# Optimization experiments

Measured on AMD Instinct MI355X. Metric: run time of the kernel, lower is better.

## Reference

```python
import jax, jax.numpy as jnp
import numpy as np

D_MODEL = 1024
N_HEADS = 16
D_KEYS = 64
D_LLM = 4096
Q_RANK = 512
KV_RANK = 512
EPS = 1e-5


def layernorm(x, g, b):
    mu = jnp.mean(x, axis=-1, keepdims=True)
    var = jnp.mean(jnp.square(x - mu), axis=-1, keepdims=True)
    return (x - mu) * jax.lax.rsqrt(var + EPS) * g + b


def setup_inputs() -> dict:
    key = jax.random.key(0)
    ks = jax.random.split(key, 10)
    te = jax.random.normal(ks[0], (4, 1024, D_MODEL), jnp.float32)
    se = jax.random.normal(ks[1], (1000, D_LLM), jnp.float32)
    s = 0.02
    return {
        'target_embedding': te,
        'source_embedding': se,
        'value_embedding': se,  # module asserts source == value
        'q_a_w': jax.random.normal(ks[2], (Q_RANK, D_MODEL), jnp.float32) * s,
        'q_ln_g': jnp.ones((Q_RANK,), jnp.float32),
        'q_ln_b': jnp.zeros((Q_RANK,), jnp.float32),
        'q_b_w': jax.random.normal(ks[3], (N_HEADS * D_KEYS, Q_RANK), jnp.float32) * s,
        'kv_a_w': jax.random.normal(ks[4], (KV_RANK, D_LLM), jnp.float32) * s,
        'kv_ln_g': jnp.ones((KV_RANK,), jnp.float32),
        'kv_ln_b': jnp.zeros((KV_RANK,), jnp.float32),
        'kv_b_w': jax.random.normal(ks[5], (N_HEADS * 2 * D_KEYS, KV_RANK), jnp.float32) * s,
        'out_w': jax.random.normal(ks[6], (D_LLM, N_HEADS * D_KEYS), jnp.float32) * s,
        'out_b': jnp.zeros((D_LLM,), jnp.float32),
    }


def reference(target_embedding, source_embedding, value_embedding,
              q_a_w, q_ln_g, q_ln_b, q_b_w,
              kv_a_w, kv_ln_g, kv_ln_b, kv_b_w, out_w, out_b):
    B, L, _ = target_embedding.shape
    S = source_embedding.shape[0]
    # Q path: LoRA down -> LN -> up, [B,L,H,E]
    q = layernorm(target_embedding @ q_a_w.T, q_ln_g, q_ln_b) @ q_b_w.T
    q = q.reshape(B, L, N_HEADS, D_KEYS)
    # KV path (no batch dim, broadcast across B)
    ckv = layernorm(source_embedding @ kv_a_w.T, kv_ln_g, kv_ln_b)  # [S, r]
    kv = (ckv @ kv_b_w.T).reshape(S, N_HEADS, 2 * D_KEYS)
    k, v = kv[..., :D_KEYS], kv[..., D_KEYS:]  # [S,H,E] each
    scale = 1.0 / np.sqrt(D_KEYS)
    scores = jnp.einsum('blhe,she->bhls', q, k)  # [B,H,L,S]
    A = jax.nn.softmax(scale * scores, axis=-1)  # dropout inactive (eval)
    out = jnp.einsum('bhls,she->blhe', A, v).reshape(B, L, N_HEADS * D_KEYS)
    return out @ out_w.T + out_b
```

## Files before the change

kernel.cpp:

```cpp
#include <hip/hip_runtime.h>

typedef unsigned short u16;
typedef __bf16 bf16x8 __attribute__((ext_vector_type(8)));
typedef float f32x4 __attribute__((ext_vector_type(4)));

#define DEV __device__ __forceinline__

DEV u16 f2bf(float f){
  unsigned u = __float_as_uint(f);
  u += 0x7fff + ((u >> 16) & 1);
  return (u16)(u >> 16);
}
DEV float bf2f(u16 v){ return __uint_as_float(((unsigned)v) << 16); }

DEV void gll16(const void* g, void* l){
  __builtin_amdgcn_global_load_lds(
    (__attribute__((address_space(1))) unsigned int*)(unsigned long long)g,
    (__attribute__((address_space(3))) unsigned int*)(unsigned int)(unsigned long long)l,
    16, 0, 0);
}

template<int WM, int WN, int OBF, int BIAS>
__global__ __launch_bounds__(256) void gemm_bt(
    const u16* __restrict__ A, int lda, long sA1, long sA2,
    const u16* __restrict__ B, int ldb, long sB1, long sB2,
    void* __restrict__ Cv, int ldc, long sC1, long sC2,
    const float* __restrict__ bias,
    int M, int N, int K, int Z2)
{
  constexpr int BM = WM*64, BN = WN*64;
  constexpr int NW = WM*WN;
  constexpr int A_INSTS = BM/16, B_INSTS = BN/16;
  constexpr int APW = A_INSTS/NW, BPW = B_INSTS/NW;
  __shared__ u16 sA[BM*32];
  __shared__ u16 sB[BN*32];
  const int tid  = threadIdx.x;
  const int wave = tid >> 6, lane = tid & 63;
  const int quad = lane >> 4, l16 = lane & 15;
  const int wm = wave % WM, wn = wave / WM;
  const long bm = blockIdx.y, bn = blockIdx.x;
  const int z  = blockIdx.z;
  const int z1 = z / Z2, z2 = z - z1*Z2;
  const u16* Ab = A + z1*sA1 + z2*sA2 + bm*BM*(long)lda;
  const u16* Bb = B + z1*sB1 + z2*sB2 + bn*BN*(long)ldb;

  f32x4 acc[4][4] = {};

  for (int k0 = 0; k0 < K; k0 += 32){
    __syncthreads();
#pragma unroll
    for (int j = 0; j < APW; j++){
      const int inst = wave*APW + j;
      const int o = inst*1024 + lane*16;
      const int row = o >> 6, colb = o & 63;
      gll16(Ab + (long)row*lda + k0 + (colb >> 1), &sA[inst*512]);
    }
#pragma unroll
    for (int j = 0; j < BPW; j++){
      const int inst = wave*BPW + j;
      const int o = inst*1024 + lane*16;
      const int row = o >> 6, colb = o & 63;
      gll16(Bb + (long)row*ldb + k0 + (colb >> 1), &sB[inst*512]);
    }
    __syncthreads();
    bf16x8 af[4], bfr[4];
#pragma unroll
    for (int mi = 0; mi < 4; mi++)
      af[mi] = *(const bf16x8*)&sA[(wm*64 + mi*16 + l16)*32 + quad*8];
#pragma unroll
    for (int ni = 0; ni < 4; ni++)
      bfr[ni] = *(const bf16x8*)&sB[(wn*64 + ni*16 + l16)*32 + quad*8];
#pragma unroll
    for (int mi = 0; mi < 4; mi++)
#pragma unroll
      for (int ni = 0; ni < 4; ni++)
        acc[mi][ni] = __builtin_amdgcn_mfma_f32_16x16x32_bf16(af[mi], bfr[ni], acc[mi][ni], 0, 0, 0);
  }

  const long crow0 = bm*BM + wm*64 + quad*4;
  const long ccol0 = bn*BN + wn*64 + l16;
  if (OBF){
    u16* Cp = (u16*)Cv + z1*sC1 + z2*sC2;
#pragma unroll
    for (int mi = 0; mi < 4; mi++)
#pragma unroll
      for (int ni = 0; ni < 4; ni++)
#pragma unroll
        for (int r = 0; r < 4; r++)
          Cp[(crow0 + mi*16 + r)*ldc + ccol0 + ni*16] = f2bf(acc[mi][ni][r]);
  } else {
    float* Cp = (float*)Cv + z1*sC1 + z2*sC2;
    float bv[4] = {0.f,0.f,0.f,0.f};
    if (BIAS){
#pragma unroll
      for (int ni = 0; ni < 4; ni++) bv[ni] = bias[ccol0 + ni*16];
    }
#pragma unroll
    for (int mi = 0; mi < 4; mi++)
#pragma unroll
      for (int ni = 0; ni < 4; ni++)
#pragma unroll
        for (int r = 0; r < 4; r++)
          Cp[(crow0 + mi*16 + r)*ldc + ccol0 + ni*16] = acc[mi][ni][r] + bv[ni];
  }
}

__global__ __launch_bounds__(512, 2) void gemm256(
    const u16* __restrict__ A, const u16* __restrict__ B,
    float* __restrict__ C, const float* __restrict__ bias,
    int N, int K, int TN)
{
  __shared__ __align__(16) u16 sA[32768];
  __shared__ __align__(16) u16 sB[32768];
  const int tid  = threadIdx.x;
  const int w    = tid >> 6, lane = tid & 63;
  const int quad = lane >> 4, l16 = lane & 15;
  const int wm = w >> 2, wn = w & 3;
  const int cpx = gridDim.x >> 3;
  const int bid = blockIdx.x;
  const int wg  = (bid & 7)*cpx + (bid >> 3);
  const long bm = wg / TN, bn = wg % TN;
  const int NT = K >> 6;

  const int rsub = lane >> 3;
  const int kk16 = (lane & 7) ^ rsub;
  const u16* Ag = A + (bm*256 + w*8 + rsub)*(long)K + kk16*8;
  const u16* Bg = B + (bn*256 + w*8 + rsub)*(long)K + kk16*8;
  u16* dA = sA + w*512;
  u16* dB = sB + w*512;

  auto stage = [&](const u16* G, u16* D, int T){
#pragma unroll
    for (int c = 0; c < 4; c++)
      gll16(G + ((long)c*64)*K + T*64, D + c*4096);
  };

  const int xr  = l16 & 7;
  const int ko0 = ((0*4 + quad) ^ xr) * 8;
  const int ko1 = ((1*4 + quad) ^ xr) * 8;
  const u16* rA0 = sA + (wm*128 + l16)*64;
  const u16* rB0 = sB + (wn*64  + l16)*64;

  f32x4 acc[8][4] = {};
  bf16x8 aF[4][2];

  stage(Ag, dA, 0);
  stage(Bg, dB, 0);
  asm volatile("s_waitcnt vmcnt(0)" ::: "memory");
  __builtin_amdgcn_s_barrier();

  for (int T = 0; T < NT; ++T){
    const int buf = T & 1;
    const u16* rA = rA0 + buf*16384;
    const u16* rB = rB0 + buf*16384;

    {
#pragma unroll
      for (int mi = 0; mi < 4; mi++){
        aF[mi][0] = *(const bf16x8*)(rA + mi*1024 + ko0);
        aF[mi][1] = *(const bf16x8*)(rA + mi*1024 + ko1);
      }
      bf16x8 bF[2][2];
#pragma unroll
      for (int ni = 0; ni < 2; ni++){
        bF[ni][0] = *(const bf16x8*)(rB + ni*1024 + ko0);
        bF[ni][1] = *(const bf16x8*)(rB + ni*1024 + ko1);
      }
      if (T+1 < NT){
        stage(Ag, dA + (buf^1)*16384, T+1);
        stage(Bg, dB + (buf^1)*16384, T+1);
      }
      __builtin_amdgcn_s_barrier();
      asm volatile("s_waitcnt lgkmcnt(0)" ::: "memory");
      __builtin_amdgcn_sched_barrier(0);
      __builtin_amdgcn_s_setprio(1);
#pragma unroll
      for (int kk = 0; kk < 2; kk++)
#pragma unroll
        for (int mi = 0; mi < 4; mi++)
#pragma unroll
          for (int ni = 0; ni < 2; ni++)
            acc[mi][ni] = __builtin_amdgcn_mfma_f32_16x16x32_bf16(aF[mi][kk], bF[ni][kk], acc[mi][ni], 0,0,0);
      __builtin_amdgcn_s_setprio(0);
      __builtin_amdgcn_s_barrier();
    }

    {
      bf16x8 bF[2][2];
#pragma unroll
      for (int ni = 0; ni < 2; ni++){
        bF[ni][0] = *(const bf16x8*)(rB + (2+ni)*1024 + ko0);
        bF[ni][1] = *(const bf16x8*)(rB + (2+ni)*1024 + ko1);
      }
      __builtin_amdgcn_s_barrier();
      asm volatile("s_waitcnt lgkmcnt(0)" ::: "memory");
      __builtin_amdgcn_sched_barrier(0);
      __builtin_amdgcn_s_setprio(1);
#pragma unroll
      for (int kk = 0; kk < 2; kk++)
#pragma unroll
        for (int mi = 0; mi < 4; mi++)
#pragma unroll
          for (int ni = 0; ni < 2; ni++)
            acc[mi][2+ni] = __builtin_amdgcn_mfma_f32_16x16x32_bf16(aF[mi][kk], bF[ni][kk], acc[mi][2+ni], 0,0,0);
      __builtin_amdgcn_s_setprio(0);
      __builtin_amdgcn_s_barrier();
    }

    {
#pragma unroll
      for (int mi = 0; mi < 4; mi++){
        aF[mi][0] = *(const bf16x8*)(rA + (4+mi)*1024 + ko0);
        aF[mi][1] = *(const bf16x8*)(rA + (4+mi)*1024 + ko1);
      }
      bf16x8 bF[2][2];
#pragma unroll
      for (int ni = 0; ni < 2; ni++){
        bF[ni][0] = *(const bf16x8*)(rB + ni*1024 + ko0);
        bF[ni][1] = *(const bf16x8*)(rB + ni*1024 + ko1);
      }
      __builtin_amdgcn_s_barrier();
      asm volatile("s_waitcnt lgkmcnt(0)" ::: "memory");
      __builtin_amdgcn_sched_barrier(0);
      __builtin_amdgcn_s_setprio(1);
#pragma unroll
      for (int kk = 0; kk < 2; kk++)
#pragma unroll
        for (int mi = 0; mi < 4; mi++)
#pragma unroll
          for (int ni = 0; ni < 2; ni++)
            acc[4+mi][ni] = __builtin_amdgcn_mfma_f32_16x16x32_bf16(aF[mi][kk], bF[ni][kk], acc[4+mi][ni], 0,0,0);
      __builtin_amdgcn_s_setprio(0);
      __builtin_amdgcn_s_barrier();
    }

    {
      bf16x8 bF[2][2];
#pragma unroll
      for (int ni = 0; ni < 2; ni++){
        bF[ni][0] = *(const bf16x8*)(rB + (2+ni)*1024 + ko0);
        bF[ni][1] = *(const bf16x8*)(rB + (2+ni)*1024 + ko1);
      }
      __builtin_amdgcn_s_barrier();
      asm volatile("s_waitcnt lgkmcnt(0)" ::: "memory");
      __builtin_amdgcn_sched_barrier(0);
      __builtin_amdgcn_s_setprio(1);
#pragma unroll
      for (int kk = 0; kk < 2; kk++)
#pragma unroll
        for (int mi = 0; mi < 4; mi++)
#pragma unroll
          for (int ni = 0; ni < 2; ni++)
            acc[4+mi][2+ni] = __builtin_amdgcn_mfma_f32_16x16x32_bf16(aF[mi][kk], bF[ni][kk], acc[4+mi][2+ni], 0,0,0);
      __builtin_amdgcn_s_setprio(0);
      asm volatile("s_waitcnt vmcnt(0)" ::: "memory");
      __builtin_amdgcn_s_barrier();
    }
  }

  const long crow0 = bm*256 + wm*128 + quad*4;
  const long ccol0 = bn*256 + wn*64  + l16;
  float bv[4];
#pragma unroll
  for (int ni = 0; ni < 4; ni++) bv[ni] = bias ? bias[ccol0 + ni*16] : 0.f;
#pragma unroll
  for (int mi = 0; mi < 8; mi++)
#pragma unroll
    for (int ni = 0; ni < 4; ni++)
#pragma unroll
      for (int r = 0; r < 4; r++)
        C[(crow0 + mi*16 + r)*(long)N + ccol0 + ni*16] = acc[mi][ni][r] + bv[ni];
}

__global__ __launch_bounds__(256) void cvt_all(
    const float* __restrict__ te,   const float* __restrict__ qaw,
    const float* __restrict__ qbw,  const float* __restrict__ kvaw,
    const float* __restrict__ kvbw, const float* __restrict__ outw,
    const float* __restrict__ se,
    u16* __restrict__ te_bf, u16* __restrict__ qa_bf, u16* __restrict__ qb_bf,
    u16* __restrict__ kva_bf, u16* __restrict__ kvb_bf,
    u16* __restrict__ outw_bf, u16* __restrict__ se_bf)
{
  const long NG = 4194304;
  for (long g = (long)blockIdx.x*256 + threadIdx.x; g < NG; g += (long)gridDim.x*256){
    const float* src; u16* dst; long rel; bool zero = false;
    if (g < 1048576)      { src=te;   dst=te_bf;   rel=g; }
    else if (g < 1179648) { src=qaw;  dst=qa_bf;   rel=g-1048576; }
    else if (g < 1310720) { src=qbw;  dst=qb_bf;   rel=g-1179648; }
    else if (g < 1835008) { src=kvaw; dst=kva_bf;  rel=g-1310720; }
    else if (g < 2097152) { src=kvbw; dst=kvb_bf;  rel=g-1835008; }
    else if (g < 3145728) { src=outw; dst=outw_bf; rel=g-2097152; }
    else                  { src=se;   dst=se_bf;   rel=g-3145728; zero = (rel>>10) >= 1000; }
    ushort4 o;
    if (!zero){
      float4 v = *(const float4*)(src + rel*4);
      o.x = f2bf(v.x); o.y = f2bf(v.y); o.z = f2bf(v.z); o.w = f2bf(v.w);
    } else { o.x = 0; o.y = 0; o.z = 0; o.w = 0; }
    *(ushort4*)(dst + rel*4) = o;
  }
}

__global__ __launch_bounds__(256) void ln_both(
    u16* __restrict__ out_q,  const float* __restrict__ in_q,
    const float* __restrict__ qg, const float* __restrict__ qb_,
    u16* __restrict__ out_kv, const float* __restrict__ in_kv,
    const float* __restrict__ kg, const float* __restrict__ kb_)
{
  long row; const float* in; u16* outp; const float* gam; const float* bet;
  int nparts; long pstride; int valid;
  if (blockIdx.x < 4096){
    row = blockIdx.x; in = in_q; outp = out_q; gam = qg; bet = qb_;
    nparts = 2; pstride = 4096L*512; valid = 1;
  } else {
    row = blockIdx.x - 4096; in = in_kv; outp = out_kv; gam = kg; bet = kb_;
    nparts = 8; pstride = 1024L*512; valid = (row < 1000);
  }
  const int tid = threadIdx.x;
  u16* op = outp + row*512 + tid*2;
  if (!valid){
    ushort2 z; z.x = 0; z.y = 0;
    *(ushort2*)op = z;
    return;
  }
  float2 x; x.x = 0.f; x.y = 0.f;
  for (int p = 0; p < nparts; p++){
    float2 v = *(const float2*)(in + p*pstride + row*512 + tid*2);
    x.x += v.x; x.y += v.y;
  }
  float s  = x.x + x.y;
  float s2 = x.x*x.x + x.y*x.y;
#pragma unroll
  for (int m = 32; m; m >>= 1){ s += __shfl_xor(s, m, 64); s2 += __shfl_xor(s2, m, 64); }
  __shared__ float red[8];
  const int wave = tid >> 6, lane = tid & 63;
  if (lane == 0){ red[wave*2] = s; red[wave*2+1] = s2; }
  __syncthreads();
  float ts = red[0]+red[2]+red[4]+red[6];
  float t2 = red[1]+red[3]+red[5]+red[7];
  float mu  = ts * (1.f/512.f);
  float var = t2 * (1.f/512.f) - mu*mu;
  float rs  = rsqrtf(var + 1e-5f);
  float2 g2 = *(const float2*)(gam + tid*2);
  float2 b2 = *(const float2*)(bet + tid*2);
  ushort2 o;
  o.x = f2bf((x.x - mu)*rs*g2.x + b2.x);
  o.y = f2bf((x.y - mu)*rs*g2.y + b2.y);
  *(ushort2*)op = o;
}

__global__ __launch_bounds__(256) void split_kv(
    const float* __restrict__ kv, u16* __restrict__ kbf, u16* __restrict__ vT)
{
  const int h  = blockIdx.x;
  const int sc = blockIdx.y;
  const int s0 = sc*64;
  const long PST = 1024L*2048;
  __shared__ u16 tile[64][65];
  const int e  = threadIdx.x & 63;
  const int sg = threadIdx.x >> 6;
#pragma unroll
  for (int i = 0; i < 16; i++){
    const int sl = i*4 + sg;
    const int s = s0 + sl;
    float kvl = kv[(long)s*2048 + h*128 + e]      + kv[PST + (long)s*2048 + h*128 + e];
    float vvl = kv[(long)s*2048 + h*128 + 64 + e] + kv[PST + (long)s*2048 + h*128 + 64 + e];
    kbf[((long)h*1024 + s)*64 + ((e + 8*s) & 63)] = f2bf(kvl);
    tile[sl][e] = f2bf(vvl);
  }
  __syncthreads();
#pragma unroll
  for (int i = 0; i < 16; i++){
    const int er = i*4 + sg;
    const int s  = s0 + e;
    const int t128 = s >> 7, pos = s & 127;
    vT[(((long)h*8 + t128)*64 + er)*128 + ((pos + 8*er) & 127)] = tile[e][er];
  }
}

__global__ __launch_bounds__(256) void flash_attn(
    const u16* __restrict__ Q, const u16* __restrict__ Kt,
    const u16* __restrict__ Vt, u16* __restrict__ O)
{
  __shared__ u16 sKV[128*64];
  __shared__ u16 sPT[128*136];
  __shared__ __align__(16) float sAl[128];
  const int tid = threadIdx.x, w = tid >> 6, lane = tid & 63;
  const int quad = lane >> 4, l16 = lane & 15;
  const int h = blockIdx.y;
  const long q0 = (long)blockIdx.x * 128;

  bf16x8 bq[2][2];
#pragma unroll
  for (int ni = 0; ni < 2; ni++)
#pragma unroll
    for (int kf = 0; kf < 2; kf++)
      bq[ni][kf] = *(const bf16x8*)&Q[(q0 + w*32 + ni*16 + l16)*1024 + h*64 + kf*32 + quad*8];

  f32x4 accO[2][4] = {};
  float mst[2] = {-3e38f, -3e38f};
  float lst[2] = {0.f, 0.f};

  for (int it = 0; it < 8; it++){
    const int s0 = it*128;
    __syncthreads();
#pragma unroll
    for (int j = 0; j < 4; j++){
      const int inst = w*4 + j;
      gll16(Kt + (long)h*65536 + (long)s0*64 + inst*512 + lane*8, &sKV[inst*512]);
    }
    __syncthreads();

    f32x4 accS[8][2] = {};
#pragma unroll
    for (int kf = 0; kf < 2; kf++)
#pragma unroll
      for (int mi = 0; mi < 8; mi++){
        const int sr = mi*16 + l16;
        bf16x8 ka = *(const bf16x8*)&sKV[sr*64 + ((kf*32 + quad*8 + 8*sr) & 63)];
#pragma unroll
        for (int ni = 0; ni < 2; ni++)
          accS[mi][ni] = __builtin_amdgcn_mfma_f32_16x16x32_bf16(ka, bq[ni][kf], accS[mi][ni], 0, 0, 0);
      }

#pragma unroll
    for (int ni = 0; ni < 2; ni++){
      float tm = -3e38f;
#pragma unroll
      for (int mi = 0; mi < 8; mi++)
#pragma unroll
        for (int r = 0; r < 4; r++){
          float v = accS[mi][ni][r] * 0.125f;
          const int s = s0 + mi*16 + quad*4 + r;
          v = (s < 1000) ? v : -3e38f;
          accS[mi][ni][r] = v;
          tm = fmaxf(tm, v);
        }
      tm = fmaxf(tm, __shfl_xor(tm, 16, 64));
      tm = fmaxf(tm, __shfl_xor(tm, 32, 64));
      const float mnew = fmaxf(mst[ni], tm);
      const float al = __expf(mst[ni] - mnew);
      mst[ni] = mnew;
      float sum = 0.f;
      const int qloc = w*32 + ni*16 + l16;
#pragma unroll
      for (int mi = 0; mi < 8; mi++){
        float p0 = __expf(accS[mi][ni][0] - mnew);
        float p1 = __expf(accS[mi][ni][1] - mnew);
        float p2 = __expf(accS[mi][ni][2] - mnew);
        float p3 = __expf(accS[mi][ni][3] - mnew);
        sum += (p0 + p1) + (p2 + p3);
        ushort4 pk;
        pk.x = f2bf(p0); pk.y = f2bf(p1); pk.z = f2bf(p2); pk.w = f2bf(p3);
        *(ushort4*)&sPT[qloc*136 + mi*16 + quad*4] = pk;
      }
      sum += __shfl_xor(sum, 16, 64);
      sum += __shfl_xor(sum, 32, 64);
      lst[ni] = lst[ni]*al + sum;
      if (quad == 0) sAl[qloc] = al;
    }
    __syncthreads();
#pragma unroll
    for (int j = 0; j < 4; j++){
      const int inst = w*4 + j;
      gll16(Vt + ((long)(h*8 + it))*8192 + inst*512 + lane*8, &sKV[inst*512]);
    }
#pragma unroll
    for (int mi = 0; mi < 2; mi++){
      f32x4 al4 = *(const f32x4*)&sAl[w*32 + mi*16 + quad*4];
#pragma unroll
      for (int ni = 0; ni < 4; ni++)
        accO[mi][ni] *= al4;
    }
    __syncthreads();

#pragma unroll
    for (int kf = 0; kf < 4; kf++){
      bf16x8 pa[2], vb[4];
#pragma unroll
      for (int mi = 0; mi < 2; mi++)
        pa[mi] = *(const bf16x8*)&sPT[(w*32 + mi*16 + l16)*136 + kf*32 + quad*8];
#pragma unroll
      for (int ni = 0; ni < 4; ni++){
        const int e = ni*16 + l16;
        vb[ni] = *(const bf16x8*)&sKV[e*128 + ((kf*32 + quad*8 + 8*e) & 127)];
      }
#pragma unroll
      for (int mi = 0; mi < 2; mi++)
#pragma unroll
        for (int ni = 0; ni < 4; ni++)
          accO[mi][ni] = __builtin_amdgcn_mfma_f32_16x16x32_bf16(pa[mi], vb[ni], accO[mi][ni], 0, 0, 0);
    }
  }

  __syncthreads();
  if (quad == 0){ sAl[w*32 + l16] = lst[0]; sAl[w*32 + 16 + l16] = lst[1]; }
  __syncthreads();
#pragma unroll
  for (int mi = 0; mi < 2; mi++){
    f32x4 l4 = *(const f32x4*)&sAl[w*32 + mi*16 + quad*4];
#pragma unroll
    for (int ni = 0; ni < 4; ni++)
#pragma unroll
      for (int r = 0; r < 4; r++)
        O[(q0 + w*32 + mi*16 + quad*4 + r)*1024 + h*64 + ni*16 + l16] =
            f2bf(accO[mi][ni][r] / l4[r]);
  }
}

extern "C" void kernel_launch(void* const* d_in, const int* in_sizes, int n_in,
                              void* d_out, int out_size, void* d_ws, size_t ws_size,
                              hipStream_t stream)
{
  const float* te   = (const float*)d_in[0];
  const float* se   = (const float*)d_in[1];
  const float* qaw  = (const float*)d_in[3];
  const float* qlg  = (const float*)d_in[4];
  const float* qlb  = (const float*)d_in[5];
  const float* qbw  = (const float*)d_in[6];
  const float* kvaw = (const float*)d_in[7];
  const float* kvlg = (const float*)d_in[8];
  const float* kvlb = (const float*)d_in[9];
  const float* kvbw = (const float*)d_in[10];
  const float* outw = (const float*)d_in[11];
  const float* outb = (const float*)d_in[12];
  float* out = (float*)d_out;
  (void)ws_size; (void)in_sizes; (void)n_in; (void)out_size;

  char* ws = (char*)d_ws;
  const size_t MB = 1024*1024;
  u16*   te_bf  = (u16*)  (ws + 0*MB);
  u16*   se_bf  = (u16*)  (ws + 8*MB);
  float* qlat   = (float*)(ws + 16*MB);
  float* ckvp   = (float*)(ws + 32*MB);
  float* kvf    = (float*)(ws + 48*MB);
  u16*   qa_bf   = (u16*)(ws + 64*MB);
  u16*   qb_bf   = (u16*)(ws + 65*MB);
  u16*   kva_bf  = (u16*)(ws + 66*MB);
  u16*   kvb_bf  = (u16*)(ws + 70*MB);
  u16*   outw_bf = (u16*)(ws + 72*MB);
  u16*   qln_bf  = (u16*)(ws + 80*MB);
  u16*   q_bf    = (u16*)(ws + 84*MB);
  u16*   ckv_bf  = (u16*)(ws + 92*MB);
  u16*   k_bf    = (u16*)(ws + 93*MB);
  u16*   vT_bf   = (u16*)(ws + 95*MB);
  u16*   attn_bf = (u16*)(ws + 97*MB);

  cvt_all<<<4096, 256, 0, stream>>>(
      te, qaw, qbw, kvaw, kvbw, outw, se,
      te_bf, qa_bf, qb_bf, kva_bf, kvb_bf, outw_bf, se_bf);

  gemm_bt<2,2,0,0><<<dim3(4, 32, 2), 256, 0, stream>>>(
      te_bf, 1024, 512, 0, qa_bf, 1024, 512, 0,
      qlat, 512, 4096L*512, 0, nullptr, 4096, 512, 512, 1);
  gemm_bt<2,2,0,0><<<dim3(4, 8, 8), 256, 0, stream>>>(
      se_bf, 4096, 512, 0, kva_bf, 4096, 512, 0,
      ckvp, 512, 1024L*512, 0, nullptr, 1024, 512, 512, 1);
  ln_both<<<4096 + 1024, 256, 0, stream>>>(
      qln_bf, qlat, qlg, qlb, ckv_bf, ckvp, kvlg, kvlb);
  gemm_bt<2,2,1,0><<<dim3(8, 32, 1), 256, 0, stream>>>(
      qln_bf, 512, 0,0, qb_bf, 512, 0,0, q_bf, 1024, 0,0, nullptr, 4096, 1024, 512, 1);
  gemm_bt<2,2,0,0><<<dim3(16, 8, 2), 256, 0, stream>>>(
      ckv_bf, 512, 256, 0, kvb_bf, 512, 256, 0,
      kvf, 2048, 1024L*2048, 0, nullptr, 1024, 2048, 256, 1);
  split_kv<<<dim3(16, 16), 256, 0, stream>>>(kvf, k_bf, vT_bf);

  flash_attn<<<dim3(32, 16), 256, 0, stream>>>(q_bf, k_bf, vT_bf, attn_bf);

  gemm256<<<dim3(256), 512, 0, stream>>>(
      attn_bf, outw_bf, out, outb, 4096, 1024, 16);
}
```

Before: 307.6 us.

## Prefetch K and V into separate LDS buffers and use exp2 softmax in attention

Splits the shared K/V staging buffer into separate sK and sV buffers. The next K tile is now loaded asynchronously during the softmax and PV phases of the current tile, and the V tile load is issued before the QK product, which removes two barriers per iteration. The softmax now uses exp2 with log2e folded into the scale, applies the sequence-length mask only on the last tile, and uses a tree max reduction with native bf16 conversion. This costs extra LDS per block and depends on the async LDS loads being properly waited on before the barriers.

After: 313.9 us. +2.0%, slower.

```diff
diff --git a/kernel.cpp b/kernel.cpp
--- a/kernel.cpp
+++ b/kernel.cpp
@@ -2,6 +2,7 @@
 
 typedef unsigned short u16;
 typedef __bf16 bf16x8 __attribute__((ext_vector_type(8)));
+typedef __bf16 bf16x4 __attribute__((ext_vector_type(4)));
 typedef float f32x4 __attribute__((ext_vector_type(4)));
 
 #define DEV __device__ __forceinline__
@@ -381,13 +382,15 @@
     const u16* __restrict__ Q, const u16* __restrict__ Kt,
     const u16* __restrict__ Vt, u16* __restrict__ O)
 {
-  __shared__ u16 sKV[128*64];
+  __shared__ u16 sK[128*64];
+  __shared__ u16 sV[64*128];
   __shared__ u16 sPT[128*136];
   __shared__ __align__(16) float sAl[128];
   const int tid = threadIdx.x, w = tid >> 6, lane = tid & 63;
   const int quad = lane >> 4, l16 = lane & 15;
   const int h = blockIdx.y;
   const long q0 = (long)blockIdx.x * 128;
+  constexpr float SC = 0.18033688011f;
 
   bf16x8 bq[2][2];
 #pragma unroll
@@ -400,15 +403,19 @@
   float mst[2] = {-3e38f, -3e38f};
   float lst[2] = {0.f, 0.f};
 
+#pragma unroll
+  for (int j = 0; j < 4; j++){
+    const int inst = w*4 + j;
+    gll16(Kt + (long)h*65536 + inst*512 + lane*8, &sK[inst*512]);
+  }
+  __syncthreads();
+
   for (int it = 0; it < 8; it++){
-    const int s0 = it*128;
-    __syncthreads();
 #pragma unroll
     for (int j = 0; j < 4; j++){
       const int inst = w*4 + j;
-      gll16(Kt + (long)h*65536 + (long)s0*64 + inst*512 + lane*8, &sKV[inst*512]);
-    }
-    __syncthreads();
+      gll16(Vt + ((long)(h*8 + it))*8192 + inst*512 + lane*8, &sV[inst*512]);
+    }
 
     f32x4 accS[8][2] = {};
 #pragma unroll
@@ -416,54 +423,71 @@
 #pragma unroll
       for (int mi = 0; mi < 8; mi++){
         const int sr = mi*16 + l16;
-        bf16x8 ka = *(const bf16x8*)&sKV[sr*64 + ((kf*32 + quad*8 + 8*sr) & 63)];
+        bf16x8 ka = *(const bf16x8*)&sK[sr*64 + ((kf*32 + quad*8 + 8*sr) & 63)];
 #pragma unroll
         for (int ni = 0; ni < 2; ni++)
           accS[mi][ni] = __builtin_amdgcn_mfma_f32_16x16x32_bf16(ka, bq[ni][kf], accS[mi][ni], 0, 0, 0);
       }
 
+    __syncthreads();
+
+    if (it < 7){
+      const long kb = (long)h*65536 + (long)(it+1)*128*64;
+#pragma unroll
+      for (int j = 0; j < 4; j++){
+        const int inst = w*4 + j;
+        gll16(Kt + kb + inst*512 + lane*8, &sK[inst*512]);
+      }
+    }
+
 #pragma unroll
     for (int ni = 0; ni < 2; ni++){
-      float tm = -3e38f;
 #pragma unroll
       for (int mi = 0; mi < 8; mi++)
 #pragma unroll
-        for (int r = 0; r < 4; r++){
-          float v = accS[mi][ni][r] * 0.125f;
-          const int s = s0 + mi*16 + quad*4 + r;
-          v = (s < 1000) ? v : -3e38f;
-          accS[mi][ni][r] = v;
-          tm = fmaxf(tm, v);
-        }
+        for (int r = 0; r < 4; r++)
+          accS[mi][ni][r] *= SC;
+      if (it == 7){
+#pragma unroll
+        for (int mi = 0; mi < 8; mi++)
+#pragma unroll
+          for (int r = 0; r < 4; r++){
+            const int s = 896 + mi*16 + quad*4 + r;
+            if (s >= 1000) accS[mi][ni][r] = -3e38f;
+          }
+      }
+      float m8[8];
+#pragma unroll
+      for (int mi = 0; mi < 8; mi++)
+        m8[mi] = fmaxf(fmaxf(accS[mi][ni][0], accS[mi][ni][1]),
+                       fmaxf(accS[mi][ni][2], accS[mi][ni][3]));
+      float tm = fmaxf(fmaxf(fmaxf(m8[0], m8[1]), fmaxf(m8[2], m8[3])),
+                       fmaxf(fmaxf(m8[4], m8[5]), fmaxf(m8[6], m8[7])));
       tm = fmaxf(tm, __shfl_xor(tm, 16, 64));
       tm = fmaxf(tm, __shfl_xor(tm, 32, 64));
       const float mnew = fmaxf(mst[ni], tm);
-      const float al = __expf(mst[ni] - mnew);
+      const float al = exp2f(mst[ni] - mnew);
       mst[ni] = mnew;
       float sum = 0.f;
       const int qloc = w*32 + ni*16 + l16;
 #pragma unroll
       for (int mi = 0; mi < 8; mi++){
-        float p0 = __expf(accS[mi][ni][0] - mnew);
-        float p1 = __expf(accS[mi][ni][1] - mnew);
-        float p2 = __expf(accS[mi][ni][2] - mnew);
-        float p3 = __expf(accS[mi][ni][3] - mnew);
+        float p0 = exp2f(accS[mi][ni][0] - mnew);
+        float p1 = exp2f(accS[mi][ni][1] - mnew);
+        float p2 = exp2f(accS[mi][ni][2] - mnew);
+        float p3 = exp2f(accS[mi][ni][3] - mnew);
         sum += (p0 + p1) + (p2 + p3);
-        ushort4 pk;
-        pk.x = f2bf(p0); pk.y = f2bf(p1); pk.z = f2bf(p2); pk.w = f2bf(p3);
-        *(ushort4*)&sPT[qloc*136 + mi*16 + quad*4] = pk;
+        bf16x4 pk;
+        pk[0] = (__bf16)p0; pk[1] = (__bf16)p1;
+        pk[2] = (__bf16)p2; pk[3] = (__bf16)p3;
+        *(bf16x4*)&sPT[qloc*136 + mi*16 + quad*4] = pk;
       }
       sum += __shfl_xor(sum, 16, 64);
       sum += __shfl_xor(sum, 32, 64);
       lst[ni] = lst[ni]*al + sum;
       if (quad == 0) sAl[qloc] = al;
     }
-    __syncthreads();
-#pragma unroll
-    for (int j = 0; j < 4; j++){
-      const int inst = w*4 + j;
-      gll16(Vt + ((long)(h*8 + it))*8192 + inst*512 + lane*8, &sKV[inst*512]);
-    }
+
 #pragma unroll
     for (int mi = 0; mi < 2; mi++){
       f32x4 al4 = *(const f32x4*)&sAl[w*32 + mi*16 + quad*4];
@@ -471,7 +495,6 @@
       for (int ni = 0; ni < 4; ni++)
         accO[mi][ni] *= al4;
     }
-    __syncthreads();
 
 #pragma unroll
     for (int kf = 0; kf < 4; kf++){
@@ -482,7 +505,7 @@
 #pragma unroll
       for (int ni = 0; ni < 4; ni++){
         const int e = ni*16 + l16;
-        vb[ni] = *(const bf16x8*)&sKV[e*128 + ((kf*32 + quad*8 + 8*e) & 127)];
+        vb[ni] = *(const bf16x8*)&sV[e*128 + ((kf*32 + quad*8 + 8*e) & 127)];
       }
 #pragma unroll
       for (int mi = 0; mi < 2; mi++)
@@ -490,11 +513,10 @@
         for (int ni = 0; ni < 4; ni++)
           accO[mi][ni] = __builtin_amdgcn_mfma_f32_16x16x32_bf16(pa[mi], vb[ni], accO[mi][ni], 0, 0, 0);
     }
-  }
-
-  __syncthreads();
+    __syncthreads();
+  }
+
   if (quad == 0){ sAl[w*32 + l16] = lst[0]; sAl[w*32 + 16 + l16] = lst[1]; }
-  __syncthreads();
 #pragma unroll
   for (int mi = 0; mi < 2; mi++){
     f32x4 l4 = *(const f32x4*)&sAl[w*32 + mi*16 + quad*4];
```
